# Kernel tuning notes

Hardware: AMD Instinct MI355X
Metric: run time of the kernel (lower is better)

Reference implementation:

```python
import jax, jax.numpy as jnp
import numpy as np
import math

D_MODEL = 1024
N_HEAD = 16
D_HEAD = D_MODEL // N_HEAD
SCALE = math.sqrt(D_HEAD)
B, S = 8, 512


def setup_inputs() -> dict:
    key = jax.random.key(0)
    ks = jax.random.split(key, 7)
    x = jax.random.normal(ks[0], (B, S, D_MODEL), dtype=jnp.float32)
    mask = jnp.ones((B, S), dtype=jnp.int32)
    qmask = jax.random.randint(ks[1], (B, S), 0, 2).astype(jnp.int32)
    # params
    Wqkv = jax.random.normal(ks[2], (4 * D_MODEL, D_MODEL), dtype=jnp.float32) / math.sqrt(D_MODEL)
    fc_w = jax.random.normal(ks[3], (D_MODEL, D_MODEL), dtype=jnp.float32) / math.sqrt(D_MODEL)
    fc_b = jnp.zeros((D_MODEL,), dtype=jnp.float32)
    shift = jnp.abs(jax.random.normal(ks[4], (1,), dtype=jnp.float32)) + 0.001
    bias = -jnp.abs(jax.random.normal(ks[5], (1,), dtype=jnp.float32))
    return {"x": x, "mask": mask, "qmask": qmask, "Wqkv": Wqkv,
            "fc_w": fc_w, "fc_b": fc_b, "shift": shift, "bias": bias}


def reference(x, mask, qmask, Wqkv, fc_w, fc_b, shift, bias):
    Bsz, L, D = x.shape
    qkv = x @ Wqkv.T  # [B,S,4D], no bias
    q, k1, k2, v = jnp.split(qkv, 4, axis=-1)

    def heads(t):  # [B,S,D] -> [B,H,S,dh]
        return t.reshape(Bsz, L, N_HEAD, D_HEAD).transpose(0, 2, 1, 3)

    q, k1, k2, v = heads(q), heads(k1), heads(k2), heads(v)

    attn_self = jnp.einsum('bhqd,bhkd->bhqk', q, k1)
    attn_others = jnp.einsum('bhqd,bhkd->bhqk', q, k2)
    same_spk = (qmask[:, :, None] == qmask[:, None, :])[:, None]  # [B,1,S,S]
    attn = jnp.where(same_spk, attn_self, attn_others) / SCALE

    # key padding mask
    attn = jnp.where((mask == 0)[:, None, None, :], -jnp.inf, attn)

    # Gaussian distance bias: -(shift*(i-j)^2 + bias)
    pos = jnp.arange(L, dtype=jnp.float32)
    sq_dist = (pos[:, None] - pos[None, :]) ** 2  # [S,S]
    attn = attn - (shift[0] * sq_dist + bias[0])

    p = jax.nn.softmax(attn, axis=-1)  # dropout=0 (eval)
    out = jnp.einsum('bhqk,bhkd->bhqd', p, v)
    out = out.transpose(0, 2, 1, 3).reshape(Bsz, L, D)
    return out @ fc_w.T + fc_b
```

## Files before the change

### kernel.cpp

```cpp
#include <hip/hip_runtime.h>

typedef unsigned short u16;
typedef __bf16 bf16_t;
typedef bf16_t bf16x8 __attribute__((ext_vector_type(8)));
typedef float f32x4 __attribute__((ext_vector_type(4)));
typedef u16 u16x8 __attribute__((ext_vector_type(8)));
typedef u16 u16x4 __attribute__((ext_vector_type(4)));

__device__ __forceinline__ u16 f2b(float f) {
    unsigned int u = __float_as_uint(f);
    u += 0x7fffu + ((u >> 16) & 1u);
    return (u16)(u >> 16);
}

__device__ __forceinline__ f32x4 mfma16(u16x8 a, u16x8 b, f32x4 c) {
    return __builtin_amdgcn_mfma_f32_16x16x32_bf16(
        __builtin_bit_cast(bf16x8, a), __builtin_bit_cast(bf16x8, b), c, 0, 0, 0);
}

#define GLDS16(gp, lp)                                                          \
    __builtin_amdgcn_global_load_lds(                                           \
        (const __attribute__((address_space(1))) void*)(gp),                    \
        (__attribute__((address_space(3))) void*)(lp), 16, 0, 0)

__global__ __launch_bounds__(256) void cvt3_kernel(const float* __restrict__ s0,
                                                   const float* __restrict__ s1,
                                                   const float* __restrict__ s2,
                                                   u16* __restrict__ d0,
                                                   u16* __restrict__ d1,
                                                   u16* __restrict__ d2) {
    int i = (blockIdx.x * 256 + threadIdx.x) * 4;
    const float* src; u16* dst;
    if (i < 4194304)       { src = s0;           dst = d0;           }
    else if (i < 8388608)  { src = s1 - 4194304; dst = d1 - 4194304; }
    else                   { src = s2 - 8388608; dst = d2 - 8388608; }
    float4 f = *(const float4*)(src + i);
    u16x4 o = { f2b(f.x), f2b(f.y), f2b(f.z), f2b(f.w) };
    *(u16x4*)(dst + i) = o;
}

template <int MT, int MODE>
__global__ __launch_bounds__(256) void gemm_bt(
    const u16* __restrict__ A, const u16* __restrict__ Bw,
    u16* __restrict__ Qf, u16* __restrict__ K1f,
    u16* __restrict__ K2f, u16* __restrict__ Vf,
    float* __restrict__ Cf, const float* __restrict__ biasp)
{
    constexpr int K = 1024;
    constexpr int MF = MT / 32;
    __shared__ u16 As[2][MT * 32];
    __shared__ u16 Bs[2][128 * 32];
    const int t = threadIdx.x;
    const int lane = t & 63;
    const int w = t >> 6;
    const int wm = w >> 1, wn = w & 1;
    const int lr = lane & 15, quad = lane >> 4;
    const int tileM = blockIdx.y * MT, tileN = blockIdx.x * 128;

    f32x4 acc[MF][4] = {};

    const u16* Ag = A + (size_t)(tileM + (t >> 2)) * K + (t & 3) * 8;
    const u16* Bg = Bw + (size_t)(tileN + (t >> 2)) * K + (t & 3) * 8;

#define STAGE(kk, bufi)                                                         \
    do {                                                                        \
        GLDS16(Ag + (kk), &As[bufi][t * 8]);                                    \
        if (MT == 128) GLDS16(Ag + (kk) + 64 * K, &As[bufi][t * 8 + 2048]);     \
        GLDS16(Bg + (kk), &Bs[bufi][t * 8]);                                    \
        GLDS16(Bg + (kk) + 64 * K, &Bs[bufi][t * 8 + 2048]);                    \
    } while (0)

    STAGE(0, 0);
    __syncthreads();

#pragma unroll 2
    for (int kk = 0; kk < K; kk += 32) {
        const int cur = (kk >> 5) & 1;
        if (kk + 32 < K) STAGE(kk + 32, cur ^ 1);

        u16x8 af[MF], bf[4];
#pragma unroll
        for (int i = 0; i < MF; ++i)
            af[i] = *(const u16x8*)(&As[cur][(wm * (MT / 2) + i * 16 + lr) * 32 + quad * 8]);
#pragma unroll
        for (int i = 0; i < 4; ++i)
            bf[i] = *(const u16x8*)(&Bs[cur][(wn * 64 + i * 16 + lr) * 32 + quad * 8]);
#pragma unroll
        for (int mi = 0; mi < MF; ++mi)
#pragma unroll
            for (int ni = 0; ni < 4; ++ni)
                acc[mi][ni] = mfma16(af[mi], bf[ni], acc[mi][ni]);

        __syncthreads();
    }
#undef STAGE

    if (MODE == 0) {
#pragma unroll
        for (int mi = 0; mi < MF; ++mi)
#pragma unroll
            for (int ni = 0; ni < 4; ++ni) {
                int n = tileN + wn * 64 + ni * 16 + lr;
                int kv = n >> 10;
                int h = (n >> 6) & 15, d = n & 63;
#pragma unroll
                for (int r = 0; r < 4; ++r) {
                    int m = tileM + wm * (MT / 2) + mi * 16 + quad * 4 + r;
                    int s = m & 511, bh = ((m >> 9) << 4) + h;
                    u16 v = f2b(acc[mi][ni][r]);
                    if (kv < 3) {
                        u16* base = (kv == 0) ? Qf : (kv == 1) ? K1f : K2f;
                        size_t idx = ((size_t)((bh * 32 + (s >> 4)) * 2 + (d >> 5))) * 512
                                   + (((d >> 3) & 3) * 16 + (s & 15)) * 8 + (d & 7);
                        base[idx] = v;
                    } else {
                        size_t idx = ((size_t)((bh * 4 + (d >> 4)) * 16 + (s >> 5))) * 512
                                   + (((s >> 3) & 3) * 16 + (d & 15)) * 8 + (s & 7);
                        Vf[idx] = v;
                    }
                }
            }
    } else {
#pragma unroll
        for (int mi = 0; mi < MF; ++mi)
#pragma unroll
            for (int ni = 0; ni < 4; ++ni) {
                int n = tileN + wn * 64 + ni * 16 + lr;
                float bv = biasp[n];
#pragma unroll
                for (int r = 0; r < 4; ++r) {
                    int m = tileM + wm * (MT / 2) + mi * 16 + quad * 4 + r;
                    Cf[(size_t)m * 1024 + n] = acc[mi][ni][r] + bv;
                }
            }
    }
}

__global__ __launch_bounds__(256) void attn_kernel(
    const u16* __restrict__ qfm, const u16* __restrict__ k1fm,
    const u16* __restrict__ k2fm, const u16* __restrict__ vfm,
    const int* __restrict__ maskp, const int* __restrict__ qmaskp,
    const float* __restrict__ shiftp, const float* __restrict__ biasp,
    u16* __restrict__ ao)
{
    __shared__ u16 Ks[2][2][2][2][512];
    __shared__ u16 Vs[2][4][512];
    __shared__ u16 Pw[4][512];

    const int bh = blockIdx.x & 127, qt = blockIdx.x >> 7;
    const int b = bh >> 4;
    const int t = threadIdx.x, lane = t & 63, w = t >> 6;
    const int lr = lane & 15, quad = lane >> 4;
    const float shiftv = shiftp[0], biasv = biasp[0];

    const int m16 = qt * 4 + w;
    const int qbase = m16 * 16;

    const u16* qsrc = qfm + ((size_t)(bh * 32 + m16) * 2) * 512 + lane * 8;
    u16x8 qa0 = *(const u16x8*)(qsrc);
    u16x8 qa1 = *(const u16x8*)(qsrc + 512);

    int qmr[4]; float rowf[4];
#pragma unroll
    for (int r = 0; r < 4; ++r) {
        int m = qbase + quad * 4 + r;
        qmr[r] = qmaskp[b * 512 + m];
        rowf[r] = (float)m;
    }

    f32x4 o0 = {0.f,0.f,0.f,0.f}, o1 = {0.f,0.f,0.f,0.f};
    f32x4 o2 = {0.f,0.f,0.f,0.f}, o3 = {0.f,0.f,0.f,0.f};
    float lsum[4] = {0.f, 0.f, 0.f, 0.f};

    u16* pbuf = &Pw[w][0];
    const int wa0 = quad * 128 + (((lr >> 3) ^ quad) * 8) + (lr & 7);
    const int wa1 = quad * 128 + (((2 | (lr >> 3)) ^ quad) * 8) + (lr & 7);
    const int ra = lr * 32 + ((quad ^ (lr >> 2)) * 8);

    const int s_ = w >> 1, kh_ = w & 1;
    const u16* k1s = k1fm + ((size_t)(bh * 32 + s_) * 2 + kh_) * 512 + lane * 8;
    const u16* k2s = k2fm + ((size_t)(bh * 32 + s_) * 2 + kh_) * 512 + lane * 8;
    const u16* vsrc = vfm + ((size_t)(bh * 4 + w) * 16) * 512 + lane * 8;

#define ASTAGE(cc, bufi)                                                        \
    do {                                                                        \
        GLDS16(k1s + (size_t)(cc) * 2048, &Ks[bufi][0][s_][kh_][lane * 8]);     \
        GLDS16(k2s + (size_t)(cc) * 2048, &Ks[bufi][1][s_][kh_][lane * 8]);     \
        GLDS16(vsrc + (size_t)(cc) * 512, &Vs[bufi][w][lane * 8]);              \
    } while (0)

    const int* qmb = qmaskp + b * 512;
    const int* kmb = maskp + b * 512;

    ASTAGE(0, 0);
    __syncthreads();

    for (int cc = 0; cc < 16; ++cc) {
        const int cur = cc & 1;
        if (cc < 15) ASTAGE(cc + 1, cur ^ 1);

        u16x8 k1t0a = *(const u16x8*)(&Ks[cur][0][0][0][lane * 8]);
        u16x8 k1t0b = *(const u16x8*)(&Ks[cur][0][0][1][lane * 8]);
        u16x8 k1t1a = *(const u16x8*)(&Ks[cur][0][1][0][lane * 8]);
        u16x8 k1t1b = *(const u16x8*)(&Ks[cur][0][1][1][lane * 8]);
        u16x8 k2t0a = *(const u16x8*)(&Ks[cur][1][0][0][lane * 8]);
        u16x8 k2t0b = *(const u16x8*)(&Ks[cur][1][0][1][lane * 8]);
        u16x8 k2t1a = *(const u16x8*)(&Ks[cur][1][1][0][lane * 8]);
        u16x8 k2t1b = *(const u16x8*)(&Ks[cur][1][1][1][lane * 8]);

        f32x4 z = {0.f, 0.f, 0.f, 0.f};
        f32x4 s1t0 = mfma16(qa1, k1t0b, mfma16(qa0, k1t0a, z));
        f32x4 s2t0 = mfma16(qa1, k2t0b, mfma16(qa0, k2t0a, z));
        f32x4 s1t1 = mfma16(qa1, k1t1b, mfma16(qa0, k1t1a, z));
        f32x4 s2t1 = mfma16(qa1, k2t1b, mfma16(qa0, k2t1a, z));

        const int col0 = cc * 32 + lr, col1 = col0 + 16;
        const int qmc0 = qmb[col0], qmc1 = qmb[col1];
        const float ka0 = (kmb[col0] ? 0.f : -1e30f) - 10.0f;
        const float ka1 = (kmb[col1] ? 0.f : -1e30f) - 10.0f;
        const float colf0 = (float)col0, colf1 = (float)col1;

        float p0[4], p1[4];
#pragma unroll
        for (int r = 0; r < 4; ++r) {
            float d0 = rowf[r] - colf0;
            float d1 = rowf[r] - colf1;
            float sel0 = (qmr[r] == qmc0) ? s1t0[r] : s2t0[r];
            float sel1 = (qmr[r] == qmc1) ? s1t1[r] : s2t1[r];
            float v0 = fmaf(sel0, 0.125f, -fmaf(shiftv * d0, d0, biasv)) + ka0;
            float v1 = fmaf(sel1, 0.125f, -fmaf(shiftv * d1, d1, biasv)) + ka1;
            p0[r] = __expf(v0);
            p1[r] = __expf(v1);
            lsum[r] += p0[r] + p1[r];
        }
#pragma unroll
        for (int r = 0; r < 4; ++r) {
            pbuf[wa0 + r * 32] = f2b(p0[r]);
            pbuf[wa1 + r * 32] = f2b(p1[r]);
        }
        u16x8 af = *(const u16x8*)(pbuf + ra);

        o0 = mfma16(af, *(const u16x8*)(&Vs[cur][0][lane * 8]), o0);
        o1 = mfma16(af, *(const u16x8*)(&Vs[cur][1][lane * 8]), o1);
        o2 = mfma16(af, *(const u16x8*)(&Vs[cur][2][lane * 8]), o2);
        o3 = mfma16(af, *(const u16x8*)(&Vs[cur][3][lane * 8]), o3);

        __syncthreads();
    }
#undef ASTAGE

#pragma unroll
    for (int r = 0; r < 4; ++r) {
        float s = lsum[r];
#pragma unroll
        for (int m = 1; m < 16; m <<= 1) s += __shfl_xor(s, m);
        float inv = 1.0f / s;
        int grow = b * 512 + qbase + quad * 4 + r;
        u16* orow = ao + (size_t)grow * 1024 + (bh & 15) * 64 + lr;
        orow[0]  = f2b(o0[r] * inv);
        orow[16] = f2b(o1[r] * inv);
        orow[32] = f2b(o2[r] * inv);
        orow[48] = f2b(o3[r] * inv);
    }
}

extern "C" void kernel_launch(void* const* d_in, const int* in_sizes, int n_in,
                              void* d_out, int out_size, void* d_ws, size_t ws_size,
                              hipStream_t stream) {
    (void)in_sizes; (void)n_in; (void)out_size; (void)ws_size;
    const float* x      = (const float*)d_in[0];
    const int*   maskp  = (const int*)d_in[1];
    const int*   qmaskp = (const int*)d_in[2];
    const float* Wqkv   = (const float*)d_in[3];
    const float* fc_w   = (const float*)d_in[4];
    const float* fc_b   = (const float*)d_in[5];
    const float* shiftp = (const float*)d_in[6];
    const float* biasp  = (const float*)d_in[7];
    float* out = (float*)d_out;

    char* ws = (char*)d_ws;
    u16* xb   = (u16*)(ws);
    u16* wb   = (u16*)(ws + (8u << 20));
    u16* fwb  = (u16*)(ws + (16u << 20));
    u16* qfm  = (u16*)(ws + (18u << 20));
    u16* k1fm = (u16*)(ws + (26u << 20));
    u16* k2fm = (u16*)(ws + (34u << 20));
    u16* vfm  = (u16*)(ws + (42u << 20));
    u16* aob  = (u16*)(ws + (50u << 20));

    cvt3_kernel<<<9216, 256, 0, stream>>>(x, Wqkv, fc_w, xb, wb, fwb);
    gemm_bt<128, 0><<<dim3(32, 32), 256, 0, stream>>>(xb, wb, qfm, k1fm, k2fm, vfm,
                                                      nullptr, nullptr);
    attn_kernel<<<1024, 256, 0, stream>>>(qfm, k1fm, k2fm, vfm, maskp, qmaskp,
                                          shiftp, biasp, aob);
    gemm_bt<64, 1><<<dim3(8, 64), 256, 0, stream>>>(aob, fwb, nullptr, nullptr,
                                                    nullptr, nullptr, out, fc_b);
}
```

Before: 203.9 us.

## Process 32 query rows per wave and load K/V directly into registers

Each wave in the attention kernel now handles two 16-row query groups, so every K/V fragment it loads feeds twice as many MFMAs, and the grid is halved to 512 blocks. The LDS double buffering through global_load_lds and the per-chunk __syncthreads are removed. K1, K2 and V fragments are read straight from global memory into registers, and only the per-wave P buffer stays in LDS. This drops block-wide barriers and LDS staging, but each of the four waves in a block now fetches the same K/V from global or cache independently. Register pressure also rises, and the number of resident blocks falls.

```diff
diff --git a/kernel.cpp b/kernel.cpp
--- a/kernel.cpp
+++ b/kernel.cpp
@@ -143,76 +143,75 @@
     const float* __restrict__ shiftp, const float* __restrict__ biasp,
     u16* __restrict__ ao)
 {
-    __shared__ u16 Ks[2][2][2][2][512];
-    __shared__ u16 Vs[2][4][512];
-    __shared__ u16 Pw[4][512];
+    __shared__ u16 Pw[4][2][512];
 
     const int bh = blockIdx.x & 127, qt = blockIdx.x >> 7;
-    const int b = bh >> 4;
+    const int b = bh >> 4, h = bh & 15;
     const int t = threadIdx.x, lane = t & 63, w = t >> 6;
     const int lr = lane & 15, quad = lane >> 4;
     const float shiftv = shiftp[0], biasv = biasp[0];
 
-    const int m16 = qt * 4 + w;
-    const int qbase = m16 * 16;
-
-    const u16* qsrc = qfm + ((size_t)(bh * 32 + m16) * 2) * 512 + lane * 8;
-    u16x8 qa0 = *(const u16x8*)(qsrc);
-    u16x8 qa1 = *(const u16x8*)(qsrc + 512);
-
-    int qmr[4]; float rowf[4];
-#pragma unroll
-    for (int r = 0; r < 4; ++r) {
-        int m = qbase + quad * 4 + r;
-        qmr[r] = qmaskp[b * 512 + m];
-        rowf[r] = (float)m;
-    }
-
-    f32x4 o0 = {0.f,0.f,0.f,0.f}, o1 = {0.f,0.f,0.f,0.f};
-    f32x4 o2 = {0.f,0.f,0.f,0.f}, o3 = {0.f,0.f,0.f,0.f};
-    float lsum[4] = {0.f, 0.f, 0.f, 0.f};
-
-    u16* pbuf = &Pw[w][0];
+    const int qbase = qt * 128 + w * 32;
+    const int m16 = qbase >> 4;
+
+    const u16* qb = qfm + ((size_t)(bh * 32 + m16) * 2) * 512 + lane * 8;
+    u16x8 qa[2][2];
+    qa[0][0] = *(const u16x8*)(qb);
+    qa[0][1] = *(const u16x8*)(qb + 512);
+    qa[1][0] = *(const u16x8*)(qb + 1024);
+    qa[1][1] = *(const u16x8*)(qb + 1536);
+
+    int qmr[2][4]; float rowf[2][4];
+#pragma unroll
+    for (int g = 0; g < 2; ++g)
+#pragma unroll
+        for (int r = 0; r < 4; ++r) {
+            int m = qbase + g * 16 + quad * 4 + r;
+            qmr[g][r] = qmaskp[b * 512 + m];
+            rowf[g][r] = (float)m;
+        }
+
+    f32x4 o[2][4] = {};
+    float lsum[2][4] = {};
+
+    u16* pb[2] = { &Pw[w][0][0], &Pw[w][1][0] };
     const int wa0 = quad * 128 + (((lr >> 3) ^ quad) * 8) + (lr & 7);
     const int wa1 = quad * 128 + (((2 | (lr >> 3)) ^ quad) * 8) + (lr & 7);
     const int ra = lr * 32 + ((quad ^ (lr >> 2)) * 8);
 
-    const int s_ = w >> 1, kh_ = w & 1;
-    const u16* k1s = k1fm + ((size_t)(bh * 32 + s_) * 2 + kh_) * 512 + lane * 8;
-    const u16* k2s = k2fm + ((size_t)(bh * 32 + s_) * 2 + kh_) * 512 + lane * 8;
-    const u16* vsrc = vfm + ((size_t)(bh * 4 + w) * 16) * 512 + lane * 8;
-
-#define ASTAGE(cc, bufi)                                                        \
-    do {                                                                        \
-        GLDS16(k1s + (size_t)(cc) * 2048, &Ks[bufi][0][s_][kh_][lane * 8]);     \
-        GLDS16(k2s + (size_t)(cc) * 2048, &Ks[bufi][1][s_][kh_][lane * 8]);     \
-        GLDS16(vsrc + (size_t)(cc) * 512, &Vs[bufi][w][lane * 8]);              \
-    } while (0)
-
+    const u16* k1b = k1fm + (size_t)bh * 32768 + lane * 8;
+    const u16* k2b = k2fm + (size_t)bh * 32768 + lane * 8;
+    const u16* vb  = vfm  + (size_t)bh * 32768 + lane * 8;
     const int* qmb = qmaskp + b * 512;
     const int* kmb = maskp + b * 512;
 
-    ASTAGE(0, 0);
-    __syncthreads();
-
+#pragma unroll 2
     for (int cc = 0; cc < 16; ++cc) {
-        const int cur = cc & 1;
-        if (cc < 15) ASTAGE(cc + 1, cur ^ 1);
-
-        u16x8 k1t0a = *(const u16x8*)(&Ks[cur][0][0][0][lane * 8]);
-        u16x8 k1t0b = *(const u16x8*)(&Ks[cur][0][0][1][lane * 8]);
-        u16x8 k1t1a = *(const u16x8*)(&Ks[cur][0][1][0][lane * 8]);
-        u16x8 k1t1b = *(const u16x8*)(&Ks[cur][0][1][1][lane * 8]);
-        u16x8 k2t0a = *(const u16x8*)(&Ks[cur][1][0][0][lane * 8]);
-        u16x8 k2t0b = *(const u16x8*)(&Ks[cur][1][0][1][lane * 8]);
-        u16x8 k2t1a = *(const u16x8*)(&Ks[cur][1][1][0][lane * 8]);
-        u16x8 k2t1b = *(const u16x8*)(&Ks[cur][1][1][1][lane * 8]);
+        const u16* kc1 = k1b + cc * 2048;
+        const u16* kc2 = k2b + cc * 2048;
+        u16x8 k1f_[2][2], k2f_[2][2];
+        k1f_[0][0] = *(const u16x8*)(kc1);
+        k1f_[0][1] = *(const u16x8*)(kc1 + 512);
+        k1f_[1][0] = *(const u16x8*)(kc1 + 1024);
+        k1f_[1][1] = *(const u16x8*)(kc1 + 1536);
+        k2f_[0][0] = *(const u16x8*)(kc2);
+        k2f_[0][1] = *(const u16x8*)(kc2 + 512);
+        k2f_[1][0] = *(const u16x8*)(kc2 + 1024);
+        k2f_[1][1] = *(const u16x8*)(kc2 + 1536);
+        u16x8 vf_[4];
+#pragma unroll
+        for (int ot = 0; ot < 4; ++ot)
+            vf_[ot] = *(const u16x8*)(vb + (size_t)(ot * 16 + cc) * 512);
 
         f32x4 z = {0.f, 0.f, 0.f, 0.f};
-        f32x4 s1t0 = mfma16(qa1, k1t0b, mfma16(qa0, k1t0a, z));
-        f32x4 s2t0 = mfma16(qa1, k2t0b, mfma16(qa0, k2t0a, z));
-        f32x4 s1t1 = mfma16(qa1, k1t1b, mfma16(qa0, k1t1a, z));
-        f32x4 s2t1 = mfma16(qa1, k2t1b, mfma16(qa0, k2t1a, z));
+        f32x4 s1[2][2], s2[2][2];
+#pragma unroll
+        for (int g = 0; g < 2; ++g)
+#pragma unroll
+            for (int tg = 0; tg < 2; ++tg) {
+                s1[g][tg] = mfma16(qa[g][1], k1f_[tg][1], mfma16(qa[g][0], k1f_[tg][0], z));
+                s2[g][tg] = mfma16(qa[g][1], k2f_[tg][1], mfma16(qa[g][0], k2f_[tg][0], z));
+            }
 
         const int col0 = cc * 32 + lr, col1 = col0 + 16;
         const int qmc0 = qmb[col0], qmc1 = qmb[col1];
@@ -220,48 +219,47 @@
         const float ka1 = (kmb[col1] ? 0.f : -1e30f) - 10.0f;
         const float colf0 = (float)col0, colf1 = (float)col1;
 
-        float p0[4], p1[4];
+#pragma unroll
+        for (int g = 0; g < 2; ++g) {
+#pragma unroll
+            for (int r = 0; r < 4; ++r) {
+                float d0 = rowf[g][r] - colf0;
+                float d1 = rowf[g][r] - colf1;
+                float sel0 = (qmr[g][r] == qmc0) ? s1[g][0][r] : s2[g][0][r];
+                float sel1 = (qmr[g][r] == qmc1) ? s1[g][1][r] : s2[g][1][r];
+                float v0 = fmaf(sel0, 0.125f, -fmaf(shiftv * d0, d0, biasv)) + ka0;
+                float v1 = fmaf(sel1, 0.125f, -fmaf(shiftv * d1, d1, biasv)) + ka1;
+                float p0 = __expf(v0);
+                float p1 = __expf(v1);
+                lsum[g][r] += p0 + p1;
+                pb[g][wa0 + r * 32] = f2b(p0);
+                pb[g][wa1 + r * 32] = f2b(p1);
+            }
+        }
+#pragma unroll
+        for (int g = 0; g < 2; ++g) {
+            u16x8 af = *(const u16x8*)(pb[g] + ra);
+#pragma unroll
+            for (int ot = 0; ot < 4; ++ot)
+                o[g][ot] = mfma16(af, vf_[ot], o[g][ot]);
+        }
+    }
+
+#pragma unroll
+    for (int g = 0; g < 2; ++g)
 #pragma unroll
         for (int r = 0; r < 4; ++r) {
-            float d0 = rowf[r] - colf0;
-            float d1 = rowf[r] - colf1;
-            float sel0 = (qmr[r] == qmc0) ? s1t0[r] : s2t0[r];
-            float sel1 = (qmr[r] == qmc1) ? s1t1[r] : s2t1[r];
-            float v0 = fmaf(sel0, 0.125f, -fmaf(shiftv * d0, d0, biasv)) + ka0;
-            float v1 = fmaf(sel1, 0.125f, -fmaf(shiftv * d1, d1, biasv)) + ka1;
-            p0[r] = __expf(v0);
-            p1[r] = __expf(v1);
-            lsum[r] += p0[r] + p1[r];
-        }
-#pragma unroll
-        for (int r = 0; r < 4; ++r) {
-            pbuf[wa0 + r * 32] = f2b(p0[r]);
-            pbuf[wa1 + r * 32] = f2b(p1[r]);
-        }
-        u16x8 af = *(const u16x8*)(pbuf + ra);
-
-        o0 = mfma16(af, *(const u16x8*)(&Vs[cur][0][lane * 8]), o0);
-        o1 = mfma16(af, *(const u16x8*)(&Vs[cur][1][lane * 8]), o1);
-        o2 = mfma16(af, *(const u16x8*)(&Vs[cur][2][lane * 8]), o2);
-        o3 = mfma16(af, *(const u16x8*)(&Vs[cur][3][lane * 8]), o3);
-
-        __syncthreads();
-    }
-#undef ASTAGE
-
-#pragma unroll
-    for (int r = 0; r < 4; ++r) {
-        float s = lsum[r];
-#pragma unroll
-        for (int m = 1; m < 16; m <<= 1) s += __shfl_xor(s, m);
-        float inv = 1.0f / s;
-        int grow = b * 512 + qbase + quad * 4 + r;
-        u16* orow = ao + (size_t)grow * 1024 + (bh & 15) * 64 + lr;
-        orow[0]  = f2b(o0[r] * inv);
-        orow[16] = f2b(o1[r] * inv);
-        orow[32] = f2b(o2[r] * inv);
-        orow[48] = f2b(o3[r] * inv);
-    }
+            float s = lsum[g][r];
+#pragma unroll
+            for (int m = 1; m < 16; m <<= 1) s += __shfl_xor(s, m);
+            float inv = 1.0f / s;
+            int grow = b * 512 + qbase + g * 16 + quad * 4 + r;
+            u16* orow = ao + (size_t)grow * 1024 + h * 64 + lr;
+            orow[0]  = f2b(o[g][0][r] * inv);
+            orow[16] = f2b(o[g][1][r] * inv);
+            orow[32] = f2b(o[g][2][r] * inv);
+            orow[48] = f2b(o[g][3][r] * inv);
+        }
 }
 
 extern "C" void kernel_launch(void* const* d_in, const int* in_sizes, int n_in,
@@ -291,8 +289,8 @@
     cvt3_kernel<<<9216, 256, 0, stream>>>(x, Wqkv, fc_w, xb, wb, fwb);
     gemm_bt<128, 0><<<dim3(32, 32), 256, 0, stream>>>(xb, wb, qfm, k1fm, k2fm, vfm,
                                                       nullptr, nullptr);
-    attn_kernel<<<1024, 256, 0, stream>>>(qfm, k1fm, k2fm, vfm, maskp, qmaskp,
-                                          shiftp, biasp, aob);
+    attn_kernel<<<512, 256, 0, stream>>>(qfm, k1fm, k2fm, vfm, maskp, qmaskp,
+                                         shiftp, biasp, aob);
     gemm_bt<64, 1><<<dim3(8, 64), 256, 0, stream>>>(aob, fwb, nullptr, nullptr,
                                                     nullptr, nullptr, out, fc_b);
 }
```

New measurement: 205.0 us. About the same (+0.6%).
